# Kernel tuning notes

Hardware: AMD Instinct MI355X
Metric: run time of the kernel (lower is better)

The kernel has to match this reference:

```python
import jax, jax.numpy as jnp
import numpy as np

HEADS = 16
DIM_HEAD = 64


def setup_inputs() -> dict:
    key = jax.random.key(0)
    k1, k2, k3 = jax.random.split(key, 3)
    b, n, dim = 4, 2048, 1024
    inner = HEADS * DIM_HEAD  # 1024
    x = jax.random.normal(k1, (b, n, dim), dtype=jnp.float32)
    # Dense weights, scaled like Glorot-ish init to keep softmax well-behaved
    w_qkv = jax.random.normal(k2, (dim, 3 * inner), dtype=jnp.float32) * (dim ** -0.5)
    w_out = jax.random.normal(k3, (inner, dim), dtype=jnp.float32) * (inner ** -0.5)
    b_out = jnp.zeros((dim,), dtype=jnp.float32)
    return {"x": x, "w_qkv": w_qkv, "w_out": w_out, "b_out": b_out}


def reference(x, w_qkv, w_out, b_out):
    b, n, dim = x.shape
    scale = DIM_HEAD ** -0.5
    qkv = x @ w_qkv  # [b, n, 3*h*d]
    q, k, v = jnp.split(qkv, 3, axis=-1)
    # 'b n (h d) -> b h n d'
    split_heads = lambda t: t.reshape(b, n, HEADS, DIM_HEAD).transpose(0, 2, 1, 3)
    q, k, v = split_heads(q), split_heads(k), split_heads(v)
    sim = jnp.einsum('bhid,bhjd->bhij', q, k) * scale  # [b, h, n, n]
    attn = jax.nn.softmax(sim, axis=-1)
    out = jnp.einsum('bhij,bhjd->bhid', attn, v)  # [b, h, n, d]
    out = out.transpose(0, 2, 1, 3).reshape(b, n, HEADS * DIM_HEAD)
    return out @ w_out + b_out  # dropout rate 0.0 -> identity
```

## Files before the change

kernel.cpp:

```cpp
#include <hip/hip_runtime.h>
#include <cstdint>

#define HEADS 16
#define DH 64
#define SEQ 2048
#define BATCH 4
#define DIM 1024
#define MTOT (BATCH*SEQ)
#define NQKV (3*DIM)

typedef short bf16x8 __attribute__((ext_vector_type(8)));
typedef float f32x4 __attribute__((ext_vector_type(4)));
typedef float f32x16 __attribute__((ext_vector_type(16)));

__device__ __forceinline__ unsigned short f2bf(float f) {
  union { float fv; unsigned int u; } c; c.fv = f;
  unsigned int u = c.u;
  u += 0x7FFFu + ((u >> 16) & 1u);
  return (unsigned short)(u >> 16);
}

__device__ __forceinline__ unsigned int pkbf(float lo, float hi) {
  union { float fv; unsigned int u; } a, b; a.fv = lo; b.fv = hi;
  return ((a.u + 0x8000u) >> 16) | ((b.u + 0x8000u) & 0xFFFF0000u);
}

__device__ __forceinline__ f32x4 mfma16(bf16x8 a, bf16x8 b, f32x4 c) {
  return __builtin_amdgcn_mfma_f32_16x16x32_bf16(a, b, c, 0, 0, 0);
}
__device__ __forceinline__ f32x16 mfma32(bf16x8 a, bf16x8 b, f32x16 c) {
  return __builtin_amdgcn_mfma_f32_32x32x16_bf16(a, b, c, 0, 0, 0);
}

typedef const __attribute__((address_space(1))) unsigned int* gas_ptr;
typedef __attribute__((address_space(3))) unsigned int* las_ptr;
__device__ __forceinline__ void gl2lds16(const void* g, void* l) {
  __builtin_amdgcn_global_load_lds((gas_ptr)g, (las_ptr)l, 16, 0, 0);
}

#define QSCALE 0.18033688011112042f

__global__ __launch_bounds__(256) void cast_f32_bf16(
    const float* __restrict__ in, unsigned short* __restrict__ out, int n4) {
  int i = blockIdx.x * blockDim.x + threadIdx.x;
  if (i >= n4) return;
  float4 v = reinterpret_cast<const float4*>(in)[i];
  uint2 o;
  o.x = (unsigned int)f2bf(v.x) | ((unsigned int)f2bf(v.y) << 16);
  o.y = (unsigned int)f2bf(v.z) | ((unsigned int)f2bf(v.w) << 16);
  reinterpret_cast<uint2*>(out)[i] = o;
}

__global__ __launch_bounds__(256) void transpose_cast(
    const float* __restrict__ in, unsigned short* __restrict__ out, int R, int C) {
  __shared__ float tile[32][33];
  int c0 = blockIdx.x * 32, r0 = blockIdx.y * 32;
  int tx = threadIdx.x & 31, ty = threadIdx.x >> 5;
  for (int i = 0; i < 32; i += 8)
    tile[ty + i][tx] = in[(size_t)(r0 + ty + i) * C + c0 + tx];
  __syncthreads();
  for (int i = 0; i < 32; i += 8)
    out[(size_t)(c0 + ty + i) * R + r0 + tx] = f2bf(tile[tx][ty + i]);
}

__global__ __launch_bounds__(256) void transpose_v(
    const unsigned short* __restrict__ V, unsigned short* __restrict__ Vt) {
  __shared__ unsigned short tile[64][72];
  int n0 = blockIdx.x * 64;
  size_t base = (size_t)blockIdx.y * SEQ * DH;
  int t = threadIdx.x;
  int r = t >> 2, c = (t & 3) * 8;
  *(uint4*)&tile[r][c]      = *(const uint4*)&V[base + (size_t)(n0 + r) * DH + c];
  *(uint4*)&tile[r][c + 32] = *(const uint4*)&V[base + (size_t)(n0 + r) * DH + c + 32];
  __syncthreads();
#pragma unroll
  for (int p = 0; p < 2; p++) {
    alignas(16) unsigned short tmp[8];
#pragma unroll
    for (int i = 0; i < 8; i++) tmp[i] = tile[c + p * 32 + i][r];
    *(uint4*)&Vt[base + (size_t)r * SEQ + n0 + c + p * 32] = *(uint4*)tmp;
  }
}

#define BM 128
#define BN 128
#define BK 32
#define LDT 32

__global__ __launch_bounds__(256) void gemm_qkv(
    const unsigned short* __restrict__ A, const unsigned short* __restrict__ Bt,
    unsigned short* __restrict__ Q, unsigned short* __restrict__ K,
    unsigned short* __restrict__ V) {
  __shared__ unsigned short sA[BM * LDT];
  __shared__ unsigned short sB[BN * LDT];
  const int KD = 1024;
  int m0 = blockIdx.y * BM;
  int n0 = blockIdx.x * BN;
  int t = threadIdx.x;
  int lane = t & 63, w = t >> 6;
  int wm = (w >> 1) * 64, wn = (w & 1) * 64;
  int fr = lane & 15, fq = (lane >> 4) * 8;

  const unsigned short* gA = &A[(size_t)(m0 + w * 16 + (lane >> 2)) * KD + (lane & 3) * 8];
  const unsigned short* gB = &Bt[(size_t)(n0 + w * 16 + (lane >> 2)) * KD + (lane & 3) * 8];
  char* lA = (char*)sA + w * 1024;
  char* lB = (char*)sB + w * 1024;

  f32x4 acc[4][4];
#pragma unroll
  for (int i = 0; i < 4; i++)
#pragma unroll
    for (int j = 0; j < 4; j++) { f32x4 z = {0.f, 0.f, 0.f, 0.f}; acc[i][j] = z; }

  for (int k0 = 0; k0 < KD; k0 += BK) {
    gl2lds16(gA + k0, lA);
    gl2lds16(gA + (size_t)64 * KD + k0, lA + 4096);
    gl2lds16(gB + k0, lB);
    gl2lds16(gB + (size_t)64 * KD + k0, lB + 4096);
    __syncthreads();
    bf16x8 af[4], bfr[4];
#pragma unroll
    for (int mt = 0; mt < 4; mt++)
      af[mt] = *reinterpret_cast<const bf16x8*>(&sA[(wm + mt * 16 + fr) * LDT + fq]);
#pragma unroll
    for (int nt = 0; nt < 4; nt++)
      bfr[nt] = *reinterpret_cast<const bf16x8*>(&sB[(wn + nt * 16 + fr) * LDT + fq]);
#pragma unroll
    for (int mt = 0; mt < 4; mt++)
#pragma unroll
      for (int nt = 0; nt < 4; nt++)
        acc[mt][nt] = mfma16(af[mt], bfr[nt], acc[mt][nt]);
    __syncthreads();
  }
  int rowq = (lane >> 4) * 4;
#pragma unroll
  for (int mt = 0; mt < 4; mt++)
#pragma unroll
    for (int nt = 0; nt < 4; nt++)
#pragma unroll
      for (int r = 0; r < 4; r++) {
        int m = m0 + wm + mt * 16 + rowq + r;
        int ncol = n0 + wn + nt * 16 + fr;
        int which = ncol >> 10;
        int hd = ncol & 1023;
        int b = m >> 11, nrow = m & 2047;
        float v = acc[mt][nt][r];
        if (which == 0) v *= QSCALE;
        unsigned short* dst = (which == 0) ? Q : (which == 1 ? K : V);
        size_t idx = ((size_t)(b * HEADS + (hd >> 6)) * SEQ + nrow) * DH + (hd & 63);
        dst[idx] = f2bf(v);
      }
}

__global__ __launch_bounds__(256) void gemm_out(
    const unsigned short* __restrict__ A, const unsigned short* __restrict__ Bt,
    const float* __restrict__ bias, float* __restrict__ C) {
  __shared__ unsigned short sA[BM * LDT];
  __shared__ unsigned short sB[BN * LDT];
  const int KD = 1024;
  int m0 = blockIdx.y * BM;
  int n0 = blockIdx.x * BN;
  int t = threadIdx.x;
  int lane = t & 63, w = t >> 6;
  int wm = (w >> 1) * 64, wn = (w & 1) * 64;
  int fr = lane & 15, fq = (lane >> 4) * 8;

  const unsigned short* gA = &A[(size_t)(m0 + w * 16 + (lane >> 2)) * KD + (lane & 3) * 8];
  const unsigned short* gB = &Bt[(size_t)(n0 + w * 16 + (lane >> 2)) * KD + (lane & 3) * 8];
  char* lA = (char*)sA + w * 1024;
  char* lB = (char*)sB + w * 1024;

  f32x4 acc[4][4];
#pragma unroll
  for (int i = 0; i < 4; i++)
#pragma unroll
    for (int j = 0; j < 4; j++) { f32x4 z = {0.f, 0.f, 0.f, 0.f}; acc[i][j] = z; }

  for (int k0 = 0; k0 < KD; k0 += BK) {
    gl2lds16(gA + k0, lA);
    gl2lds16(gA + (size_t)64 * KD + k0, lA + 4096);
    gl2lds16(gB + k0, lB);
    gl2lds16(gB + (size_t)64 * KD + k0, lB + 4096);
    __syncthreads();
    bf16x8 af[4], bfr[4];
#pragma unroll
    for (int mt = 0; mt < 4; mt++)
      af[mt] = *reinterpret_cast<const bf16x8*>(&sA[(wm + mt * 16 + fr) * LDT + fq]);
#pragma unroll
    for (int nt = 0; nt < 4; nt++)
      bfr[nt] = *reinterpret_cast<const bf16x8*>(&sB[(wn + nt * 16 + fr) * LDT + fq]);
#pragma unroll
    for (int mt = 0; mt < 4; mt++)
#pragma unroll
      for (int nt = 0; nt < 4; nt++)
        acc[mt][nt] = mfma16(af[mt], bfr[nt], acc[mt][nt]);
    __syncthreads();
  }
  int rowq = (lane >> 4) * 4;
#pragma unroll
  for (int mt = 0; mt < 4; mt++)
#pragma unroll
    for (int nt = 0; nt < 4; nt++)
#pragma unroll
      for (int r = 0; r < 4; r++) {
        int m = m0 + wm + mt * 16 + rowq + r;
        int ncol = n0 + wn + nt * 16 + fr;
        C[(size_t)m * DIM + ncol] = acc[mt][nt][r] + bias[ncol];
      }
}

#define LDA 72

__global__ __launch_bounds__(256, 2) void attention(
    const unsigned short* __restrict__ Qg, const unsigned short* __restrict__ Kg,
    const unsigned short* __restrict__ Vtg, unsigned short* __restrict__ Og) {
  __shared__ unsigned short smem[2 * 64 * LDA];
  unsigned short* sK  = smem;
  unsigned short* sVt = smem + 64 * LDA;
  int qb = blockIdx.x, h = blockIdx.y, b = blockIdx.z;
  size_t base = (size_t)(b * HEADS + h) * SEQ * DH;
  const unsigned short* Q = Qg + base;
  const unsigned short* K = Kg + base;
  const unsigned short* Vt = Vtg + base;
  int t = threadIdx.x, lane = t & 63, w = t >> 6;
  int m = lane & 31, kh = lane >> 5;
  int q0 = qb * 256 + w * 64;

  bf16x8 qf[2][4];
#pragma unroll
  for (int qh = 0; qh < 2; qh++)
#pragma unroll
    for (int kt = 0; kt < 4; kt++)
      qf[qh][kt] = *reinterpret_cast<const bf16x8*>(
          &Q[(size_t)(q0 + 32 * qh + m) * DH + kt * 16 + kh * 8]);

  f32x16 oaccT[2][2];
#pragma unroll
  for (int qh = 0; qh < 2; qh++)
#pragma unroll
    for (int dh = 0; dh < 2; dh++)
#pragma unroll
      for (int i = 0; i < 16; i++) oaccT[qh][dh][i] = 0.f;
  float rs[2] = {0.f, 0.f};

  int sr = t >> 2, sc = (t & 3) * 8;

  for (int j0 = 0; j0 < SEQ; j0 += 64) {
    *(uint4*)&sK[sr * LDA + sc]       = *(const uint4*)&K[(size_t)(j0 + sr) * DH + sc];
    *(uint4*)&sK[sr * LDA + sc + 32]  = *(const uint4*)&K[(size_t)(j0 + sr) * DH + sc + 32];
    *(uint4*)&sVt[sr * LDA + sc]      = *(const uint4*)&Vt[(size_t)sr * SEQ + j0 + sc];
    *(uint4*)&sVt[sr * LDA + sc + 32] = *(const uint4*)&Vt[(size_t)sr * SEQ + j0 + sc + 32];
    __syncthreads();

    unsigned int pp[2][8][2];
#pragma unroll
    for (int jt = 0; jt < 2; jt++) {
      bf16x8 kf[4];
#pragma unroll
      for (int kt = 0; kt < 4; kt++)
        kf[kt] = *reinterpret_cast<const bf16x8*>(
            &sK[(jt * 32 + m) * LDA + (2 * kt + kh) * 8]);
#pragma unroll
      for (int qh = 0; qh < 2; qh++) {
        f32x16 s;
#pragma unroll
        for (int i = 0; i < 16; i++) s[i] = 0.f;
#pragma unroll
        for (int kt = 0; kt < 4; kt++)
          s = mfma32(kf[kt], qf[qh][kt], s);
        float e[16];
#pragma unroll
        for (int i = 0; i < 16; i++) e[i] = __builtin_amdgcn_exp2f(s[i]);
        float t0 = (e[0] + e[1]) + (e[2] + e[3]);
        float t1 = (e[4] + e[5]) + (e[6] + e[7]);
        float t2 = (e[8] + e[9]) + (e[10] + e[11]);
        float t3 = (e[12] + e[13]) + (e[14] + e[15]);
        rs[qh] += (t0 + t1) + (t2 + t3);
#pragma unroll
        for (int sl = 0; sl < 4; sl++) {
          pp[qh][4 * jt + sl][0] = pkbf(e[4 * sl + 0], e[4 * sl + 1]);
          pp[qh][4 * jt + sl][1] = pkbf(e[4 * sl + 2], e[4 * sl + 3]);
        }
      }
    }

#pragma unroll
    for (int kb = 0; kb < 4; kb++) {
#pragma unroll
      for (int dh = 0; dh < 2; dh++) {
        union { uint2 u[2]; bf16x8 v; } ac;
        ac.u[0] = *(const uint2*)&sVt[(32 * dh + m) * LDA + 16 * kb + 4 * kh];
        ac.u[1] = *(const uint2*)&sVt[(32 * dh + m) * LDA + 16 * kb + 8 + 4 * kh];
#pragma unroll
        for (int qh = 0; qh < 2; qh++) {
          union { unsigned int u[4]; bf16x8 v; } bc;
          bc.u[0] = pp[qh][2 * kb][0];
          bc.u[1] = pp[qh][2 * kb][1];
          bc.u[2] = pp[qh][2 * kb + 1][0];
          bc.u[3] = pp[qh][2 * kb + 1][1];
          oaccT[qh][dh] = mfma32(ac.v, bc.v, oaccT[qh][dh]);
        }
      }
    }
    __syncthreads();
  }

  float inv[2];
#pragma unroll
  for (int qh = 0; qh < 2; qh++) {
    float tot = rs[qh] + __shfl_xor(rs[qh], 32);
    inv[qh] = 1.0f / tot;
  }

  unsigned int* ew = (unsigned int*)smem + (size_t)w * 32 * 36;
#pragma unroll
  for (int qh = 0; qh < 2; qh++) {
#pragma unroll
    for (int dh = 0; dh < 2; dh++)
#pragma unroll
      for (int sl = 0; sl < 4; sl++) {
        unsigned int u0 = pkbf(oaccT[qh][dh][4 * sl + 0] * inv[qh],
                               oaccT[qh][dh][4 * sl + 1] * inv[qh]);
        unsigned int u1 = pkbf(oaccT[qh][dh][4 * sl + 2] * inv[qh],
                               oaccT[qh][dh][4 * sl + 3] * inv[qh]);
        uint2 pk; pk.x = u0; pk.y = u1;
        *(uint2*)&ew[m * 36 + 16 * dh + 4 * sl + 2 * kh] = pk;
      }
    int mr = lane >> 3, ch = lane & 7;
#pragma unroll
    for (int it = 0; it < 4; it++) {
      uint4 vv = *(const uint4*)&ew[(8 * it + mr) * 36 + ch * 4];
      int n = q0 + 32 * qh + 8 * it + mr;
      *(uint4*)&Og[((size_t)(b * SEQ + n)) * DIM + h * DH + ch * 8] = vv;
    }
  }
}

extern "C" void kernel_launch(void* const* d_in, const int* in_sizes, int n_in,
                              void* d_out, int out_size, void* d_ws, size_t ws_size,
                              hipStream_t stream) {
  const float* x     = (const float*)d_in[0];
  const float* w_qkv = (const float*)d_in[1];
  const float* w_out = (const float*)d_in[2];
  const float* b_out = (const float*)d_in[3];
  float* out = (float*)d_out;

  char* ws = (char*)d_ws;
  unsigned short* xb     = (unsigned short*)ws; ws += (size_t)MTOT * DIM * 2;
  unsigned short* wqkv_t = (unsigned short*)ws; ws += (size_t)NQKV * DIM * 2;
  unsigned short* wout_t = (unsigned short*)ws; ws += (size_t)DIM * DIM * 2;
  unsigned short* qb_    = (unsigned short*)ws; ws += (size_t)BATCH * HEADS * SEQ * DH * 2;
  unsigned short* kb_    = (unsigned short*)ws; ws += (size_t)BATCH * HEADS * SEQ * DH * 2;
  unsigned short* vb_    = (unsigned short*)ws; ws += (size_t)BATCH * HEADS * SEQ * DH * 2;
  unsigned short* attnb  = (unsigned short*)ws; ws += (size_t)MTOT * DIM * 2;
  unsigned short* vt_    = xb;

  cast_f32_bf16<<<(MTOT * DIM / 4 + 255) / 256, 256, 0, stream>>>(x, xb, MTOT * DIM / 4);
  transpose_cast<<<dim3(NQKV / 32, DIM / 32), 256, 0, stream>>>(w_qkv, wqkv_t, DIM, NQKV);
  transpose_cast<<<dim3(DIM / 32, DIM / 32), 256, 0, stream>>>(w_out, wout_t, DIM, DIM);

  gemm_qkv<<<dim3(NQKV / BN, MTOT / BM), 256, 0, stream>>>(xb, wqkv_t, qb_, kb_, vb_);

  transpose_v<<<dim3(SEQ / 64, BATCH * HEADS), 256, 0, stream>>>(vb_, vt_);

  attention<<<dim3(SEQ / 256, HEADS, BATCH), 256, 0, stream>>>(qb_, kb_, vt_, attnb);

  gemm_out<<<dim3(DIM / BN, MTOT / BM), 256, 0, stream>>>(attnb, wout_t, b_out, out);
}
```

Measured before the change: 275.4 us.

## Fuse prep kernels, write V transposed from QKV GEMM, double-buffer attention tiles

Merges the input cast and both weight transpose-casts into one launch. The QKV GEMM epilogue now writes V directly in transposed layout, which removes the separate transpose_v kernel. The attention kernel gets double-buffered K/Vt shared-memory tiles with register prefetch of the next tile, so global loads overlap with the MFMA work. The costs are scattered 2-byte V stores, doubled LDS use that may limit occupancy, and extra registers held for the prefetch.

```diff
diff --git a/kernel.cpp b/kernel.cpp
--- a/kernel.cpp
+++ b/kernel.cpp
@@ -40,46 +40,42 @@
 
 #define QSCALE 0.18033688011112042f
 
-__global__ __launch_bounds__(256) void cast_f32_bf16(
-    const float* __restrict__ in, unsigned short* __restrict__ out, int n4) {
-  int i = blockIdx.x * blockDim.x + threadIdx.x;
-  if (i >= n4) return;
-  float4 v = reinterpret_cast<const float4*>(in)[i];
-  uint2 o;
-  o.x = (unsigned int)f2bf(v.x) | ((unsigned int)f2bf(v.y) << 16);
-  o.y = (unsigned int)f2bf(v.z) | ((unsigned int)f2bf(v.w) << 16);
-  reinterpret_cast<uint2*>(out)[i] = o;
-}
-
-__global__ __launch_bounds__(256) void transpose_cast(
-    const float* __restrict__ in, unsigned short* __restrict__ out, int R, int C) {
+#define CAST_BLKS (MTOT * DIM / 4 / 256)
+#define TQKV_BLKS ((NQKV / 32) * (DIM / 32))
+#define TOUT_BLKS ((DIM / 32) * (DIM / 32))
+
+__global__ __launch_bounds__(256) void prep(
+    const float* __restrict__ x, const float* __restrict__ w_qkv,
+    const float* __restrict__ w_out, unsigned short* __restrict__ xb,
+    unsigned short* __restrict__ wqkv_t, unsigned short* __restrict__ wout_t) {
   __shared__ float tile[32][33];
-  int c0 = blockIdx.x * 32, r0 = blockIdx.y * 32;
+  int blk = blockIdx.x;
+  if (blk < CAST_BLKS) {
+    int i = blk * 256 + threadIdx.x;
+    float4 v = reinterpret_cast<const float4*>(x)[i];
+    uint2 o;
+    o.x = (unsigned int)f2bf(v.x) | ((unsigned int)f2bf(v.y) << 16);
+    o.y = (unsigned int)f2bf(v.z) | ((unsigned int)f2bf(v.w) << 16);
+    reinterpret_cast<uint2*>(xb)[i] = o;
+    return;
+  }
+  blk -= CAST_BLKS;
+  const float* in; unsigned short* out; int R, C, bx, by;
+  if (blk < TQKV_BLKS) {
+    in = w_qkv; out = wqkv_t; R = DIM; C = NQKV;
+    bx = blk % (NQKV / 32); by = blk / (NQKV / 32);
+  } else {
+    blk -= TQKV_BLKS;
+    in = w_out; out = wout_t; R = DIM; C = DIM;
+    bx = blk % (DIM / 32); by = blk / (DIM / 32);
+  }
+  int c0 = bx * 32, r0 = by * 32;
   int tx = threadIdx.x & 31, ty = threadIdx.x >> 5;
   for (int i = 0; i < 32; i += 8)
     tile[ty + i][tx] = in[(size_t)(r0 + ty + i) * C + c0 + tx];
   __syncthreads();
   for (int i = 0; i < 32; i += 8)
     out[(size_t)(c0 + ty + i) * R + r0 + tx] = f2bf(tile[tx][ty + i]);
-}
-
-__global__ __launch_bounds__(256) void transpose_v(
-    const unsigned short* __restrict__ V, unsigned short* __restrict__ Vt) {
-  __shared__ unsigned short tile[64][72];
-  int n0 = blockIdx.x * 64;
-  size_t base = (size_t)blockIdx.y * SEQ * DH;
-  int t = threadIdx.x;
-  int r = t >> 2, c = (t & 3) * 8;
-  *(uint4*)&tile[r][c]      = *(const uint4*)&V[base + (size_t)(n0 + r) * DH + c];
-  *(uint4*)&tile[r][c + 32] = *(const uint4*)&V[base + (size_t)(n0 + r) * DH + c + 32];
-  __syncthreads();
-#pragma unroll
-  for (int p = 0; p < 2; p++) {
-    alignas(16) unsigned short tmp[8];
-#pragma unroll
-    for (int i = 0; i < 8; i++) tmp[i] = tile[c + p * 32 + i][r];
-    *(uint4*)&Vt[base + (size_t)r * SEQ + n0 + c + p * 32] = *(uint4*)tmp;
-  }
 }
 
 #define BM 128
@@ -146,9 +142,13 @@
         int b = m >> 11, nrow = m & 2047;
         float v = acc[mt][nt][r];
         if (which == 0) v *= QSCALE;
-        unsigned short* dst = (which == 0) ? Q : (which == 1 ? K : V);
-        size_t idx = ((size_t)(b * HEADS + (hd >> 6)) * SEQ + nrow) * DH + (hd & 63);
-        dst[idx] = f2bf(v);
+        int bh = b * HEADS + (hd >> 6), d = hd & 63;
+        if (which == 2) {
+          V[((size_t)bh * DH + d) * SEQ + nrow] = f2bf(v);
+        } else {
+          unsigned short* dst = (which == 0) ? Q : K;
+          dst[((size_t)bh * SEQ + nrow) * DH + d] = f2bf(v);
+        }
       }
 }
 
@@ -210,13 +210,12 @@
 }
 
 #define LDA 72
+#define TBUF (64 * LDA)
 
 __global__ __launch_bounds__(256, 2) void attention(
     const unsigned short* __restrict__ Qg, const unsigned short* __restrict__ Kg,
     const unsigned short* __restrict__ Vtg, unsigned short* __restrict__ Og) {
-  __shared__ unsigned short smem[2 * 64 * LDA];
-  unsigned short* sK  = smem;
-  unsigned short* sVt = smem + 64 * LDA;
+  __shared__ unsigned short smem[4 * TBUF];
   int qb = blockIdx.x, h = blockIdx.y, b = blockIdx.z;
   size_t base = (size_t)(b * HEADS + h) * SEQ * DH;
   const unsigned short* Q = Qg + base;
@@ -245,12 +244,31 @@
 
   int sr = t >> 2, sc = (t & 3) * 8;
 
-  for (int j0 = 0; j0 < SEQ; j0 += 64) {
-    *(uint4*)&sK[sr * LDA + sc]       = *(const uint4*)&K[(size_t)(j0 + sr) * DH + sc];
-    *(uint4*)&sK[sr * LDA + sc + 32]  = *(const uint4*)&K[(size_t)(j0 + sr) * DH + sc + 32];
-    *(uint4*)&sVt[sr * LDA + sc]      = *(const uint4*)&Vt[(size_t)sr * SEQ + j0 + sc];
-    *(uint4*)&sVt[sr * LDA + sc + 32] = *(const uint4*)&Vt[(size_t)sr * SEQ + j0 + sc + 32];
-    __syncthreads();
+  {
+    uint4 rk0 = *(const uint4*)&K[(size_t)sr * DH + sc];
+    uint4 rk1 = *(const uint4*)&K[(size_t)sr * DH + sc + 32];
+    uint4 rv0 = *(const uint4*)&Vt[(size_t)sr * SEQ + sc];
+    uint4 rv1 = *(const uint4*)&Vt[(size_t)sr * SEQ + sc + 32];
+    *(uint4*)&smem[sr * LDA + sc]              = rk0;
+    *(uint4*)&smem[sr * LDA + sc + 32]         = rk1;
+    *(uint4*)&smem[TBUF + sr * LDA + sc]       = rv0;
+    *(uint4*)&smem[TBUF + sr * LDA + sc + 32]  = rv1;
+  }
+  __syncthreads();
+
+  for (int ti = 0; ti < SEQ / 64; ti++) {
+    int cur = ti & 1;
+    const unsigned short* cK = smem + cur * 2 * TBUF;
+    const unsigned short* cV = cK + TBUF;
+    bool more = (ti + 1) < SEQ / 64;
+    uint4 rk0, rk1, rv0, rv1;
+    if (more) {
+      int j1 = (ti + 1) * 64;
+      rk0 = *(const uint4*)&K[(size_t)(j1 + sr) * DH + sc];
+      rk1 = *(const uint4*)&K[(size_t)(j1 + sr) * DH + sc + 32];
+      rv0 = *(const uint4*)&Vt[(size_t)sr * SEQ + j1 + sc];
+      rv1 = *(const uint4*)&Vt[(size_t)sr * SEQ + j1 + sc + 32];
+    }
 
     unsigned int pp[2][8][2];
 #pragma unroll
@@ -259,7 +277,7 @@
 #pragma unroll
       for (int kt = 0; kt < 4; kt++)
         kf[kt] = *reinterpret_cast<const bf16x8*>(
-            &sK[(jt * 32 + m) * LDA + (2 * kt + kh) * 8]);
+            &cK[(jt * 32 + m) * LDA + (2 * kt + kh) * 8]);
 #pragma unroll
       for (int qh = 0; qh < 2; qh++) {
         f32x16 s;
@@ -289,8 +307,8 @@
 #pragma unroll
       for (int dh = 0; dh < 2; dh++) {
         union { uint2 u[2]; bf16x8 v; } ac;
-        ac.u[0] = *(const uint2*)&sVt[(32 * dh + m) * LDA + 16 * kb + 4 * kh];
-        ac.u[1] = *(const uint2*)&sVt[(32 * dh + m) * LDA + 16 * kb + 8 + 4 * kh];
+        ac.u[0] = *(const uint2*)&cV[(32 * dh + m) * LDA + 16 * kb + 4 * kh];
+        ac.u[1] = *(const uint2*)&cV[(32 * dh + m) * LDA + 16 * kb + 8 + 4 * kh];
 #pragma unroll
         for (int qh = 0; qh < 2; qh++) {
           union { unsigned int u[4]; bf16x8 v; } bc;
@@ -302,6 +320,15 @@
         }
       }
     }
+
+    if (more) {
+      unsigned short* nK = smem + (1 - cur) * 2 * TBUF;
+      unsigned short* nV = nK + TBUF;
+      *(uint4*)&nK[sr * LDA + sc]      = rk0;
+      *(uint4*)&nK[sr * LDA + sc + 32] = rk1;
+      *(uint4*)&nV[sr * LDA + sc]      = rv0;
+      *(uint4*)&nV[sr * LDA + sc + 32] = rv1;
+    }
     __syncthreads();
   }
 
@@ -351,19 +378,15 @@
   unsigned short* wout_t = (unsigned short*)ws; ws += (size_t)DIM * DIM * 2;
   unsigned short* qb_    = (unsigned short*)ws; ws += (size_t)BATCH * HEADS * SEQ * DH * 2;
   unsigned short* kb_    = (unsigned short*)ws; ws += (size_t)BATCH * HEADS * SEQ * DH * 2;
-  unsigned short* vb_    = (unsigned short*)ws; ws += (size_t)BATCH * HEADS * SEQ * DH * 2;
+  unsigned short* vtb    = (unsigned short*)ws; ws += (size_t)BATCH * HEADS * SEQ * DH * 2;
   unsigned short* attnb  = (unsigned short*)ws; ws += (size_t)MTOT * DIM * 2;
-  unsigned short* vt_    = xb;
-
-  cast_f32_bf16<<<(MTOT * DIM / 4 + 255) / 256, 256, 0, stream>>>(x, xb, MTOT * DIM / 4);
-  transpose_cast<<<dim3(NQKV / 32, DIM / 32), 256, 0, stream>>>(w_qkv, wqkv_t, DIM, NQKV);
-  transpose_cast<<<dim3(DIM / 32, DIM / 32), 256, 0, stream>>>(w_out, wout_t, DIM, DIM);
-
-  gemm_qkv<<<dim3(NQKV / BN, MTOT / BM), 256, 0, stream>>>(xb, wqkv_t, qb_, kb_, vb_);
-
-  transpose_v<<<dim3(SEQ / 64, BATCH * HEADS), 256, 0, stream>>>(vb_, vt_);
-
-  attention<<<dim3(SEQ / 256, HEADS, BATCH), 256, 0, stream>>>(qb_, kb_, vt_, attnb);
+
+  prep<<<CAST_BLKS + TQKV_BLKS + TOUT_BLKS, 256, 0, stream>>>(
+      x, w_qkv, w_out, xb, wqkv_t, wout_t);
+
+  gemm_qkv<<<dim3(NQKV / BN, MTOT / BM), 256, 0, stream>>>(xb, wqkv_t, qb_, kb_, vtb);
+
+  attention<<<dim3(SEQ / 256, HEADS, BATCH), 256, 0, stream>>>(qb_, kb_, vtb, attnb);
 
   gemm_out<<<dim3(DIM / BN, MTOT / BM), 256, 0, stream>>>(attnb, wout_t, b_out, out);
 }
```

Result: slower. 281.4 us (+2.2%).
